# Kernel tuning notes

Hardware: AMD Instinct MI355X
Metric: run time of the kernel (lower is better)

Reference implementation:

```python
import jax, jax.numpy as jnp
import numpy as np

EPS = 1e-8

def setup_inputs() -> dict:
    key = jax.random.key(0)
    k1, k2 = jax.random.split(key)
    B, C, H, W = 8, 21, 512, 512
    inp = jax.random.normal(k1, (B, C, H, W), dtype=jnp.float32)
    target = jax.random.uniform(k2, (B, C, H, W), dtype=jnp.float32)
    return {"input": inp, "target": target}

def reference(input, target):
    B, C, H, W = input.shape
    # argmax over class dim -> [B, H, W]
    pred = jnp.argmax(input, axis=1)
    # one-hot of prediction, flattened over spatial dims -> [B, HW, C]
    h = jax.nn.one_hot(pred.reshape(B, H * W), C, dtype=input.dtype)
    # target flattened over spatial dims -> [B, C, HW]
    y = target.reshape(B, C, H * W)
    # cm[b, i, j] = sum_n y[b, i, n] * h[b, n, j]  -> [B, C, C]
    cm = jnp.einsum('bin,bnj->bij', y, h)
    # row-normalize by target mass per class, then mean over batch -> [C, C]
    cm = cm / (jnp.sum(y, axis=2, keepdims=True) + EPS)
    return jnp.mean(cm, axis=0)
```

## Files before the change

### kernel.cpp

```cpp
#include <hip/hip_runtime.h>

#define NC 21
#define NB 8
#define HW (512*512)
#define EPS 1e-8f

__global__ __launch_bounds__(256) void cm_accum(const float* __restrict__ input,
                                                const float* __restrict__ target,
                                                float* __restrict__ cm ) {
    __shared__ float scm[NC * NC];
    const int t = threadIdx.x;
    for (int i = t; i < NC * NC; i += 256) scm[i] = 0.0f;
    __syncthreads();

    const int b    = blockIdx.x >> 8;
    const int tile = blockIdx.x & 255;
    const int q    = (tile << 8) + t;

    const float4* ip = (const float4*)(input  + (size_t)b * NC * HW);
    const float4* tp = (const float4*)(target + (size_t)b * NC * HW);
    const int plane4 = HW / 4;

    float4 m = ip[q];
    int jx = 0, jy = 0, jz = 0, jw = 0;
    #pragma unroll
    for (int c = 1; c < NC; ++c) {
        float4 v = ip[c * plane4 + q];
        if (v.x > m.x) { m.x = v.x; jx = c; }
        if (v.y > m.y) { m.y = v.y; jy = c; }
        if (v.z > m.z) { m.z = v.z; jz = c; }
        if (v.w > m.w) { m.w = v.w; jw = c; }
    }

    #pragma unroll
    for (int i = 0; i < NC; ++i) {
        float4 y = tp[i * plane4 + q];
        const int row = i * NC;
        atomicAdd(&scm[row + jx], y.x);
        atomicAdd(&scm[row + jy], y.y);
        atomicAdd(&scm[row + jz], y.z);
        atomicAdd(&scm[row + jw], y.w);
    }
    __syncthreads();

    for (int i = t; i < NC * NC; i += 256) atomicAdd(&cm[b * NC * NC + i], scm[i]);
}

__global__ __launch_bounds__(512) void cm_final(const float* __restrict__ cm,
                                                float* __restrict__ out) {
    __shared__ float rs[NB * NC];
    const int t = threadIdx.x;
    if (t < NB * NC) {
        const int b = t / NC, i = t % NC;
        float s = 0.0f;
        for (int j = 0; j < NC; ++j) s += cm[b * NC * NC + i * NC + j];
        rs[t] = s + EPS;
    }
    __syncthreads();
    if (t < NC * NC) {
        const int i = t / NC;
        float acc = 0.0f;
        for (int b = 0; b < NB; ++b) acc += cm[b * NC * NC + t] / rs[b * NC + i];
        out[t] = acc * (1.0f / NB);
    }
}

extern "C" void kernel_launch(void* const* d_in, const int* in_sizes, int n_in,
                              void* d_out, int out_size, void* d_ws, size_t ws_size,
                              hipStream_t stream) {
    const float* input  = (const float*)d_in[0];
    const float* target = (const float*)d_in[1];
    float* out = (float*)d_out;
    float* cm  = (float*)d_ws;

    hipMemsetAsync(cm, 0, NB * NC * NC * sizeof(float), stream);
    cm_accum<<<NB * 256, 256, 0, stream>>>(input, target, cm);
    cm_final<<<1, 512, 0, stream>>>(cm, out);
}
```

Measured before the change: 495.7 us.

## Batch channel loads in groups of seven and replicate shared histograms

```diff
diff --git a/kernel.cpp b/kernel.cpp
--- a/kernel.cpp
+++ b/kernel.cpp
@@ -8,9 +8,9 @@
 __global__ __launch_bounds__(256) void cm_accum(const float* __restrict__ input,
                                                 const float* __restrict__ target,
                                                 float* __restrict__ cm ) {
-    __shared__ float scm[NC * NC];
+    __shared__ float scm[4][NC * NC];
     const int t = threadIdx.x;
-    for (int i = t; i < NC * NC; i += 256) scm[i] = 0.0f;
+    for (int i = t; i < 4 * NC * NC; i += 256) ((float*)scm)[i] = 0.0f;
     __syncthreads();
 
     const int b    = blockIdx.x >> 8;
@@ -21,29 +21,59 @@
     const float4* tp = (const float4*)(target + (size_t)b * NC * HW);
     const int plane4 = HW / 4;
 
-    float4 m = ip[q];
+    float4 m;
     int jx = 0, jy = 0, jz = 0, jw = 0;
-    #pragma unroll
-    for (int c = 1; c < NC; ++c) {
-        float4 v = ip[c * plane4 + q];
-        if (v.x > m.x) { m.x = v.x; jx = c; }
-        if (v.y > m.y) { m.y = v.y; jy = c; }
-        if (v.z > m.z) { m.z = v.z; jz = c; }
-        if (v.w > m.w) { m.w = v.w; jw = c; }
+    {
+        float4 v[7];
+        #pragma unroll
+        for (int u = 0; u < 7; ++u) v[u] = ip[u * plane4 + q];
+        m = v[0];
+        #pragma unroll
+        for (int u = 1; u < 7; ++u) {
+            if (v[u].x > m.x) { m.x = v[u].x; jx = u; }
+            if (v[u].y > m.y) { m.y = v[u].y; jy = u; }
+            if (v[u].z > m.z) { m.z = v[u].z; jz = u; }
+            if (v[u].w > m.w) { m.w = v[u].w; jw = u; }
+        }
+    }
+    #pragma unroll 1
+    for (int g = 1; g < 3; ++g) {
+        float4 v[7];
+        const int c0 = g * 7;
+        #pragma unroll
+        for (int u = 0; u < 7; ++u) v[u] = ip[(c0 + u) * plane4 + q];
+        #pragma unroll
+        for (int u = 0; u < 7; ++u) {
+            const int c = c0 + u;
+            if (v[u].x > m.x) { m.x = v[u].x; jx = c; }
+            if (v[u].y > m.y) { m.y = v[u].y; jy = c; }
+            if (v[u].z > m.z) { m.z = v[u].z; jz = c; }
+            if (v[u].w > m.w) { m.w = v[u].w; jw = c; }
+        }
     }
 
-    #pragma unroll
-    for (int i = 0; i < NC; ++i) {
-        float4 y = tp[i * plane4 + q];
-        const int row = i * NC;
-        atomicAdd(&scm[row + jx], y.x);
-        atomicAdd(&scm[row + jy], y.y);
-        atomicAdd(&scm[row + jz], y.z);
-        atomicAdd(&scm[row + jw], y.w);
+    float* my = scm[(t >> 4) & 3];
+    #pragma unroll 1
+    for (int g = 0; g < 3; ++g) {
+        float4 y[7];
+        const int c0 = g * 7;
+        #pragma unroll
+        for (int u = 0; u < 7; ++u) y[u] = tp[(c0 + u) * plane4 + q];
+        #pragma unroll
+        for (int u = 0; u < 7; ++u) {
+            const int row = (c0 + u) * NC;
+            atomicAdd(&my[row + jx], y[u].x);
+            atomicAdd(&my[row + jy], y[u].y);
+            atomicAdd(&my[row + jz], y[u].z);
+            atomicAdd(&my[row + jw], y[u].w);
+        }
     }
     __syncthreads();
 
-    for (int i = t; i < NC * NC; i += 256) atomicAdd(&cm[b * NC * NC + i], scm[i]);
+    for (int i = t; i < NC * NC; i += 256) {
+        const float s = scm[0][i] + scm[1][i] + scm[2][i] + scm[3][i];
+        atomicAdd(&cm[b * NC * NC + i], s);
+    }
 }
 
 __global__ __launch_bounds__(512) void cm_final(const float* __restrict__ cm,
```

Measured after the change: 487.0 us. Within noise of the previous version (-1.7%).

## Batch all class loads upfront and replicate shared histograms to cut atomic contention

Applied to the files above, without the earlier changes.

```diff
diff --git a/kernel.cpp b/kernel.cpp
--- a/kernel.cpp
+++ b/kernel.cpp
@@ -4,13 +4,14 @@
 #define NB 8
 #define HW (512*512)
 #define EPS 1e-8f
+#define NREP 8
 
 __global__ __launch_bounds__(256) void cm_accum(const float* __restrict__ input,
                                                 const float* __restrict__ target,
                                                 float* __restrict__ cm ) {
-    __shared__ float scm[NC * NC];
+    __shared__ float scm[NREP][NC * NC];
     const int t = threadIdx.x;
-    for (int i = t; i < NC * NC; i += 256) scm[i] = 0.0f;
+    for (int i = t; i < NREP * NC * NC; i += 256) ((float*)scm)[i] = 0.0f;
     __syncthreads();
 
     const int b    = blockIdx.x >> 8;
@@ -21,29 +22,43 @@
     const float4* tp = (const float4*)(target + (size_t)b * NC * HW);
     const int plane4 = HW / 4;
 
-    float4 m = ip[q];
+    float4 v[NC];
+    #pragma unroll
+    for (int c = 0; c < NC; ++c) v[c] = ip[c * plane4 + q];
+    __builtin_amdgcn_sched_barrier(0);
+
+    float4 m = v[0];
     int jx = 0, jy = 0, jz = 0, jw = 0;
     #pragma unroll
     for (int c = 1; c < NC; ++c) {
-        float4 v = ip[c * plane4 + q];
-        if (v.x > m.x) { m.x = v.x; jx = c; }
-        if (v.y > m.y) { m.y = v.y; jy = c; }
-        if (v.z > m.z) { m.z = v.z; jz = c; }
-        if (v.w > m.w) { m.w = v.w; jw = c; }
+        if (v[c].x > m.x) { m.x = v[c].x; jx = c; }
+        if (v[c].y > m.y) { m.y = v[c].y; jy = c; }
+        if (v[c].z > m.z) { m.z = v[c].z; jz = c; }
+        if (v[c].w > m.w) { m.w = v[c].w; jw = c; }
     }
 
+    float4 y[NC];
     #pragma unroll
-    for (int i = 0; i < NC; ++i) {
-        float4 y = tp[i * plane4 + q];
-        const int row = i * NC;
-        atomicAdd(&scm[row + jx], y.x);
-        atomicAdd(&scm[row + jy], y.y);
-        atomicAdd(&scm[row + jz], y.z);
-        atomicAdd(&scm[row + jw], y.w);
+    for (int c = 0; c < NC; ++c) y[c] = tp[c * plane4 + q];
+    __builtin_amdgcn_sched_barrier(0);
+
+    float* my = scm[t & (NREP - 1)];
+    #pragma unroll
+    for (int c = 0; c < NC; ++c) {
+        const int row = c * NC;
+        atomicAdd(&my[row + jx], y[c].x);
+        atomicAdd(&my[row + jy], y[c].y);
+        atomicAdd(&my[row + jz], y[c].z);
+        atomicAdd(&my[row + jw], y[c].w);
     }
     __syncthreads();
 
-    for (int i = t; i < NC * NC; i += 256) atomicAdd(&cm[b * NC * NC + i], scm[i]);
+    for (int i = t; i < NC * NC; i += 256) {
+        float s = 0.0f;
+        #pragma unroll
+        for (int r = 0; r < NREP; ++r) s += scm[r][i];
+        atomicAdd(&cm[b * NC * NC + i], s);
+    }
 }
 
 __global__ __launch_bounds__(512) void cm_final(const float* __restrict__ cm,
```

Measured after the change: 502.7 us. No clear change (+1.4%).
